# Optimization experiments

Hardware: AMD Instinct MI355X
Metric: run time of the kernel (lower is better)

Reference implementation:

```python
import jax, jax.numpy as jnp
import numpy as np

D_MODEL = 1024
HEADS = 16
D_K = D_MODEL // HEADS
B, S = 2, 2048


def setup_inputs() -> dict:
    key = jax.random.key(0)
    ks = jax.random.split(key, 11)
    sc = 1.0 / np.sqrt(D_MODEL)
    return {
        "q": jax.random.normal(ks[0], (B, S, D_MODEL), jnp.float32),
        "k": jax.random.normal(ks[1], (B, S, D_MODEL), jnp.float32),
        "v": jax.random.normal(ks[2], (B, S, D_MODEL), jnp.float32),
        "Wq": jax.random.normal(ks[3], (D_MODEL, D_MODEL), jnp.float32) * sc,
        "bq": jnp.zeros((D_MODEL,), jnp.float32),
        "Wk": jax.random.normal(ks[4], (D_MODEL, D_MODEL), jnp.float32) * sc,
        "bk": jnp.zeros((D_MODEL,), jnp.float32),
        "Wv": jax.random.normal(ks[5], (D_MODEL, D_MODEL), jnp.float32) * sc,
        "bv": jnp.zeros((D_MODEL,), jnp.float32),
        "Wo": jax.random.normal(ks[6], (D_MODEL, D_MODEL), jnp.float32) * sc,
        "bo": jnp.zeros((D_MODEL,), jnp.float32),
    }


def reference(q, k, v, Wq, bq, Wk, bk, Wv, bv, Wo, bo):
    bs = q.shape[0]
    # linear projections then split heads: [B,S,D] -> [B,H,S,Dk]
    def proj(x, W, b):
        y = x @ W.T + b
        return y.reshape(bs, -1, HEADS, D_K).transpose(0, 2, 1, 3)

    qh = proj(q, Wq, bq)
    kh = proj(k, Wk, bk)
    vh = proj(v, Wv, bv)
    # scores: [B,H,Sq,Sk] -- full attention matrix as in the original
    scores = jnp.einsum("bhqd,bhkd->bhqk", qh, kh) / jnp.sqrt(
        jnp.asarray(D_K, jnp.float32))
    attn = jax.nn.softmax(scores, axis=-1)
    # dropout is identity in eval/reference mode
    out = jnp.einsum("bhqk,bhkd->bhqd", attn, vh)
    concat = out.transpose(0, 2, 1, 3).reshape(bs, -1, D_MODEL)
    return concat @ Wo.T + bo
```

## Files before the change

### kernel.cpp

```cpp
#include <hip/hip_runtime.h>
#include <hip/hip_bf16.h>

typedef __attribute__((ext_vector_type(8))) short bf16x8;
typedef __attribute__((ext_vector_type(4))) float f32x4;
typedef __attribute__((ext_vector_type(16))) float f32x16;

#define DM   1024
#define SEQ  2048
#define NB   2
#define NH   16
#define MR   (NB*SEQ)

#define SMK  (MR*DM)
#define W1M  (DM*DM)

#define QSCALE 0.18033688011112042f

#define OFF_QB  ((size_t)0)
#define OFF_KB  ((size_t)SMK)
#define OFF_WQB ((size_t)(3*(size_t)SMK))
#define OFF_WO  ((size_t)(3*(size_t)SMK + 3*(size_t)W1M))
#define OFF_QP  ((size_t)(3*(size_t)SMK + 4*(size_t)W1M))
#define OFF_KP  ((size_t)(4*(size_t)SMK + 4*(size_t)W1M))
#define OFF_VP  ((size_t)(5*(size_t)SMK + 4*(size_t)W1M))
#define OFF_CC  ((size_t)0)

__device__ __forceinline__ unsigned short f2bf(float f) {
  union { __hip_bfloat16 b; unsigned short u; } cv;
  cv.b = __float2bfloat16(f);
  return cv.u;
}

__device__ __forceinline__ unsigned int cvtpk_bf16(float lo, float hi) {
  unsigned int r;
  asm("v_cvt_pk_bf16_f32 %0, %1, %2" : "=v"(r) : "v"(lo), "v"(hi));
  return r;
}

__device__ __forceinline__ void plane32_swap(unsigned int& a, unsigned int& b) {
  asm("v_permlane32_swap_b32 %0, %1" : "+v"(a), "+v"(b));
}

__global__ __launch_bounds__(256) void cvt_all(const float* __restrict__ wq,
                                               const float* __restrict__ wk,
                                               const float* __restrict__ wo,
                                               const float* __restrict__ v,
                                               unsigned short* __restrict__ ws) {
  int i = blockIdx.x * 256 + threadIdx.x;
  const float* src;
  unsigned short* dst;
  int j;
  if (i < 3 * (W1M / 4)) {
    int z = i >> 18;
    j = i & ((W1M / 4) - 1);
    src = (z == 0) ? wq : ((z == 1) ? wk : wo);
    dst = ws + ((z == 2) ? OFF_WO : OFF_WQB + (size_t)z * W1M);
  } else {
    j = i - 3 * (W1M / 4);
    src = v;
    dst = ws + OFF_KB;
  }
  float4 val = reinterpret_cast<const float4*>(src)[j];
  ushort4 o;
  o.x = f2bf(val.x); o.y = f2bf(val.y); o.z = f2bf(val.z); o.w = f2bf(val.w);
  reinterpret_cast<ushort4*>(dst)[j] = o;
}

__device__ __forceinline__ void gload_lds16(const void* g, void* l) {
  __builtin_amdgcn_global_load_lds(
      (const __attribute__((address_space(1))) unsigned int*)g,
      (__attribute__((address_space(3))) unsigned int*)l,
      16, 0, 0);
}

template<bool BIAS_ROW>
__device__ __forceinline__ void gemm_hyb2_body(unsigned short* __restrict__ As,
                                               unsigned short* __restrict__ Bs,
                                               const float* __restrict__ A,
                                               const unsigned short* __restrict__ B,
                                               const float* __restrict__ bias,
                                               unsigned short* __restrict__ C,
                                               int N, int K, float scale,
                                               int brow, int bcol) {
  const int tid  = threadIdx.x;
  const int lane = tid & 63;
  const int w    = tid >> 6;
  const int wr   = w >> 1, wc = w & 1;

  f32x4 acc[4][4];
#pragma unroll
  for (int m = 0; m < 4; m++)
#pragma unroll
    for (int n = 0; n < 4; n++) acc[m][n] = (f32x4){0.f, 0.f, 0.f, 0.f};

  const int srow = lane >> 2;
  const int scol = (lane & 3) * 8;

  f32x4 ra0[2][2], ra1[2][2];

  auto loadA = [&](int k0, f32x4 (&fa)[2][2]) {
#pragma unroll
    for (int i = 0; i < 2; i++) {
      const float* pa = A + (size_t)(brow + (w + i * 4) * 16 + srow) * K + k0 + scol;
      fa[i][0] = *(const f32x4*)pa;
      fa[i][1] = *(const f32x4*)(pa + 4);
    }
  };
  auto commitA = [&](int buf, f32x4 (&fa)[2][2]) {
#pragma unroll
    for (int i = 0; i < 2; i++) {
      union { unsigned int u[4]; bf16x8 v8; } ua;
#pragma unroll
      for (int j = 0; j < 2; j++) {
        ua.u[2 * j]     = cvtpk_bf16(fa[i][j][0], fa[i][j][1]);
        ua.u[2 * j + 1] = cvtpk_bf16(fa[i][j][2], fa[i][j][3]);
      }
      *(bf16x8*)((char*)As + (size_t)buf * 8192 + (w + i * 4) * 1024 + lane * 16) = ua.v8;
    }
  };
  auto stageB = [&](int buf, int k0) {
#pragma unroll
    for (int c = w; c < 8; c += 4)
      gload_lds16(B + (size_t)(bcol + c * 16 + srow) * K + k0 + scol,
                  (char*)Bs + (size_t)buf * 8192 + c * 1024);
  };

  const int nk = K / 32;

  loadA(0, ra0);
  commitA(0, ra0);
  loadA(32, ra1);
  stageB(0, 0);
  loadA(64, ra0);

  const int lrow_a = wr * 64 + (lane & 15);
  const int lrow_b = wc * 64 + (lane & 15);
  const int lcol   = (lane >> 4) * 8;

  auto iter = [&](int kt, f32x4 (&rs)[2][2]) {
    if (kt + 2 < nk) asm volatile("s_waitcnt vmcnt(4) lgkmcnt(0)" ::: "memory");
    else             asm volatile("s_waitcnt vmcnt(0) lgkmcnt(0)" ::: "memory");
    __builtin_amdgcn_s_barrier();
    __builtin_amdgcn_sched_barrier(0);
    int buf = kt & 1;
    bf16x8 a[4], b[4];
#pragma unroll
    for (int m = 0; m < 4; m++)
      a[m] = *(const bf16x8*)&As[(size_t)buf * 4096 + (lrow_a + m * 16) * 32 + lcol];
#pragma unroll
    for (int n = 0; n < 4; n++)
      b[n] = *(const bf16x8*)&Bs[(size_t)buf * 4096 + (lrow_b + n * 16) * 32 + lcol];
    if (kt + 1 < nk) {
      commitA(buf ^ 1, rs);
      stageB(buf ^ 1, (kt + 1) * 32);
    }
    if (kt + 3 < nk) loadA((kt + 3) * 32, rs);
    __builtin_amdgcn_s_setprio(1);
#pragma unroll
    for (int m = 0; m < 4; m++)
#pragma unroll
      for (int n = 0; n < 4; n++)
        acc[m][n] = __builtin_amdgcn_mfma_f32_16x16x32_bf16(a[m], b[n], acc[m][n], 0, 0, 0);
    __builtin_amdgcn_s_setprio(0);
  };

  for (int kt = 0; kt < nk; kt += 2) {
    iter(kt,     ra1);
    iter(kt + 1, ra0);
  }

  const int crow0 = brow + wr * 64;
  const int ccol0 = bcol + wc * 64;
  const int rsub  = (lane >> 4) * 4;
  const int csub  = lane & 15;
#pragma unroll
  for (int m = 0; m < 4; m++)
#pragma unroll
    for (int n = 0; n < 4; n++) {
      int col = ccol0 + n * 16 + csub;
      float bcol_v = BIAS_ROW ? 0.f : bias[col];
#pragma unroll
      for (int qq = 0; qq < 4; qq++) {
        int row = crow0 + m * 16 + rsub + qq;
        float bb = BIAS_ROW ? bias[row] : bcol_v;
        C[(size_t)row * N + col] = f2bf((acc[m][n][qq] + bb) * scale);
      }
    }
}

__global__ __launch_bounds__(256, 3) void gemm_qkv(const float* __restrict__ q,
                                                   const float* __restrict__ k,
                                                   const float* __restrict__ Wv,
                                                   unsigned short* ws,
                                                   const float* __restrict__ bq,
                                                   const float* __restrict__ bk,
                                                   const float* __restrict__ bv) {
  __shared__ unsigned short As[2 * 128 * 32];
  __shared__ unsigned short Bs[2 * 128 * 32];
  const int i  = blockIdx.x;
  const int x  = i & 7;
  const int r  = i >> 3;
  const int pm = r >> 3;
  const int bx = r & 7;
  const int p  = x * 12 + pm;
  const int z  = p >> 5;
  const int by = p & 31;
  if (z < 2) {
    gemm_hyb2_body<false>(As, Bs,
                          z ? k : q, ws + OFF_WQB + (size_t)z * W1M, z ? bk : bq,
                          ws + OFF_QP + (size_t)z * SMK,
                          DM, DM, z ? 1.f : QSCALE, by * 128, bx * 128);
  } else {
    gemm_hyb2_body<true>(As, Bs,
                         Wv, ws + OFF_KB, bv,
                         ws + OFF_VP,
                         MR, DM, 1.f, bx * 128, by * 128);
  }
}

__device__ __forceinline__ void gemm_out_body(unsigned short* __restrict__ As,
                                              unsigned short* __restrict__ Bs,
                                              const unsigned short* __restrict__ A,
                                              const unsigned short* __restrict__ Bt,
                                              const float* __restrict__ bias,
                                              float* __restrict__ Cv,
                                              int N, int K,
                                              int brow, int bcol) {
  constexpr int BM = 64, BN = 128;
  const int tid  = threadIdx.x;
  const int lane = tid & 63;
  const int w    = tid >> 6;
  const int wr   = w >> 1, wc = w & 1;

  f32x4 acc[2][4];
#pragma unroll
  for (int m = 0; m < 2; m++)
#pragma unroll
    for (int n = 0; n < 4; n++) acc[m][n] = (f32x4){0.f, 0.f, 0.f, 0.f};

  const int srow = lane >> 2;
  const int scol = (lane & 3) * 8;

  auto stage = [&](int buf, int k0) {
#pragma unroll
    for (int c = w; c < BM / 16; c += 4)
      gload_lds16(A + (size_t)(brow + c * 16 + srow) * K + k0 + scol,
                  (char*)As + (size_t)buf * BM * 64 + c * 1024);
#pragma unroll
    for (int c = w; c < BN / 16; c += 4)
      gload_lds16(Bt + (size_t)(bcol + c * 16 + srow) * K + k0 + scol,
                  (char*)Bs + (size_t)buf * BN * 64 + c * 1024);
  };

  stage(0, 0);
  stage(1, 32);

  const int nk = K / 32;
  const int lrow_a = wr * (BM / 2) + (lane & 15);
  const int lrow_b = wc * (BN / 2) + (lane & 15);
  const int lcol   = (lane >> 4) * 8;

  int b0 = 0;
  for (int kt = 0; kt < nk; ++kt) {
    if (kt + 1 < nk) asm volatile("s_waitcnt vmcnt(3)" ::: "memory");
    else             asm volatile("s_waitcnt vmcnt(0)" ::: "memory");
    __builtin_amdgcn_s_barrier();
    __builtin_amdgcn_sched_barrier(0);
    if (kt + 2 < nk) {
      int bn = b0 + 2; if (bn >= 3) bn -= 3;
      stage(bn, (kt + 2) * 32);
    }
    bf16x8 a[2], b[4];
#pragma unroll
    for (int m = 0; m < 2; m++)
      a[m] = *(const bf16x8*)&As[(size_t)b0 * BM * 32 + (lrow_a + m * 16) * 32 + lcol];
#pragma unroll
    for (int n = 0; n < 4; n++)
      b[n] = *(const bf16x8*)&Bs[(size_t)b0 * BN * 32 + (lrow_b + n * 16) * 32 + lcol];
    __builtin_amdgcn_s_setprio(1);
#pragma unroll
    for (int m = 0; m < 2; m++)
#pragma unroll
      for (int n = 0; n < 4; n++)
        acc[m][n] = __builtin_amdgcn_mfma_f32_16x16x32_bf16(a[m], b[n], acc[m][n], 0, 0, 0);
    __builtin_amdgcn_s_setprio(0);
    b0 = (b0 == 2) ? 0 : b0 + 1;
  }

  const int crow0 = brow + wr * (BM / 2);
  const int ccol0 = bcol + wc * (BN / 2);
  const int rsub  = (lane >> 4) * 4;
  const int csub  = lane & 15;
#pragma unroll
  for (int m = 0; m < 2; m++)
#pragma unroll
    for (int n = 0; n < 4; n++) {
      int col = ccol0 + n * 16 + csub;
      float bv = bias[col];
#pragma unroll
      for (int qq = 0; qq < 4; qq++) {
        int row = crow0 + m * 16 + rsub + qq;
        Cv[(size_t)row * N + col] = acc[m][n][qq] + bv;
      }
    }
}

__global__ __launch_bounds__(256) void gemm_out(const unsigned short* __restrict__ ws,
                                                const float* __restrict__ bo,
                                                float* __restrict__ out) {
  __shared__ unsigned short As[3 * 64 * 32];
  __shared__ unsigned short Bs[3 * 128 * 32];
  const int i  = blockIdx.x;
  const int x  = i & 7;
  const int r  = i >> 3;
  const int pm = r >> 3;
  const int bx = r & 7;
  const int by = x * 8 + pm;
  gemm_out_body(As, Bs,
                ws + OFF_CC, ws + OFF_WO, bo, out,
                DM, DM, by * 64, bx * 128);
}

__global__ __launch_bounds__(512, 4) void flash_attn(unsigned short* ws) {
  __shared__ __align__(16) unsigned char smem[65536];

  const int tid  = threadIdx.x;
  const int lane = tid & 63;
  const int w    = tid >> 6;
  const int s    = w >> 2;
  const int wsub = w & 3;
  const int q    = lane & 31;
  const int hi   = lane >> 5;
  const int swq  = q & 7;
  const int bid  = blockIdx.x;
  const int swzb = (bid & 7) * 64 + (bid >> 3);
  const int qblk = swzb & 15;
  const int bh   = swzb >> 4;
  const int b    = bh >> 4, h = bh & 15;

  const unsigned short* Qp = ws + OFF_QP;
  const unsigned short* Kp = ws + OFF_KP;
  const unsigned short* Vp = ws + OFF_VP;
  unsigned short* CC = ws + OFF_CC;

  const unsigned short* Kg = Kp + (size_t)(b * SEQ) * DM + h * 64;
  const unsigned short* Vg = Vp + (size_t)(h * 64) * MR + (size_t)b * SEQ;

  bf16x8 bqf[4];
  {
    const unsigned short* qrow =
        Qp + (size_t)(b * SEQ + qblk * 128 + wsub * 32 + q) * DM + h * 64;
#pragma unroll
    for (int c = 0; c < 4; c++)
      bqf[c] = *(const bf16x8*)(qrow + c * 16 + hi * 8);
  }

  f32x16 o_acc[2];
#pragma unroll
  for (int dt = 0; dt < 2; dt++)
#pragma unroll
    for (int r = 0; r < 16; r++) o_acc[dt][r] = 0.f;
  float l_run = 0.f;

  auto stage = [&](int buf, int t) {
    const unsigned short* Kt = Kg + (size_t)(s * 16 + t) * 64 * DM;
    const unsigned short* Vt = Vg + (s * 16 + t) * 64;
    char* base = (char*)smem + (size_t)(s * 2 + buf) * 16384;
#pragma unroll
    for (int i = 0; i < 2; i++) {
      int slot = wsub * 128 + i * 64 + lane;
      int srow = slot >> 3;
      int gch  = (slot & 7) ^ (srow & 7);
      gload_lds16(Kt + (size_t)srow * DM + gch * 8, base + slot * 16);
      gload_lds16(Vt + (size_t)srow * MR + gch * 8, base + 8192 + slot * 16);
    }
  };

  stage(0, 0);

  for (int t = 0; t < 16; ++t) {
    int buf = t & 1;
    __syncthreads();
    if (t + 1 < 16) stage(buf ^ 1, t + 1);
    const unsigned short* Kb = (const unsigned short*)(smem + (size_t)(s * 2 + buf) * 16384);
    const unsigned short* Vb = Kb + 4096;

    f32x16 st0, st1;
#pragma unroll
    for (int r = 0; r < 16; r++) { st0[r] = 0.f; st1[r] = 0.f; }
    __builtin_amdgcn_s_setprio(1);
#pragma unroll
    for (int c = 0; c < 4; c++) {
      int ch = (((c << 1) | hi) ^ swq) << 3;
      bf16x8 ak0 = *(const bf16x8*)&Kb[q * 64 + ch];
      bf16x8 ak1 = *(const bf16x8*)&Kb[(32 + q) * 64 + ch];
      st0 = __builtin_amdgcn_mfma_f32_32x32x16_bf16(ak0, bqf[c], st0, 0, 0, 0);
      st1 = __builtin_amdgcn_mfma_f32_32x32x16_bf16(ak1, bqf[c], st1, 0, 0, 0);
    }
    __builtin_amdgcn_s_setprio(0);

    unsigned int pk0[8], pk1[8];
    float lt = 0.f;
#pragma unroll
    for (int p = 0; p < 8; p++) {
      float a0 = __builtin_amdgcn_exp2f(st0[2 * p]);
      float a1 = __builtin_amdgcn_exp2f(st0[2 * p + 1]);
      float b0 = __builtin_amdgcn_exp2f(st1[2 * p]);
      float b1 = __builtin_amdgcn_exp2f(st1[2 * p + 1]);
      lt += (a0 + a1) + (b0 + b1);
      pk0[p] = cvtpk_bf16(a0, a1);
      pk1[p] = cvtpk_bf16(b0, b1);
    }
    l_run += lt;

    plane32_swap(pk0[0], pk0[2]); plane32_swap(pk0[1], pk0[3]);
    plane32_swap(pk0[4], pk0[6]); plane32_swap(pk0[5], pk0[7]);
    plane32_swap(pk1[0], pk1[2]); plane32_swap(pk1[1], pk1[3]);
    plane32_swap(pk1[4], pk1[6]); plane32_swap(pk1[5], pk1[7]);

    __builtin_amdgcn_s_setprio(1);
#pragma unroll
    for (int t4 = 0; t4 < 4; t4++) {
      union { unsigned int u[4]; bf16x8 v; } pb;
      const unsigned int* src = (t4 < 2) ? pk0 : pk1;
      pb.u[0] = src[(t4 & 1) * 4 + 0];
      pb.u[1] = src[(t4 & 1) * 4 + 1];
      pb.u[2] = src[(t4 & 1) * 4 + 2];
      pb.u[3] = src[(t4 & 1) * 4 + 3];
      int ch = (((t4 << 1) | hi) ^ swq) << 3;
#pragma unroll
      for (int dt = 0; dt < 2; dt++) {
        bf16x8 av = *(const bf16x8*)&Vb[(dt * 32 + q) * 64 + ch];
        o_acc[dt] = __builtin_amdgcn_mfma_f32_32x32x16_bf16(av, pb.v, o_acc[dt], 0, 0, 0);
      }
    }
    __builtin_amdgcn_s_setprio(0);
  }

  __syncthreads();
  float* scr = (float*)smem;
  float lsum = l_run + __shfl_xor(l_run, 32, 64);
  if (s == 1) {
    int idx = (wsub * 64 + lane) * 33;
#pragma unroll
    for (int dt = 0; dt < 2; dt++)
#pragma unroll
      for (int r = 0; r < 16; r++) scr[idx + dt * 16 + r] = o_acc[dt][r];
    scr[idx + 32] = lsum;
  }
  __syncthreads();
  if (s == 0) {
    int idx = (wsub * 64 + lane) * 33;
#pragma unroll
    for (int dt = 0; dt < 2; dt++)
#pragma unroll
      for (int r = 0; r < 16; r++) o_acc[dt][r] += scr[idx + dt * 16 + r];
    float l = lsum + scr[idx + 32];
    float inv = 1.f / l;

    int qg = b * SEQ + qblk * 128 + wsub * 32 + q;
    unsigned short* crow = CC + (size_t)qg * DM + h * 64;
#pragma unroll
    for (int dt = 0; dt < 2; dt++)
#pragma unroll
      for (int rq = 0; rq < 4; rq++) {
        ushort4 o;
        o.x = f2bf(o_acc[dt][4 * rq + 0] * inv);
        o.y = f2bf(o_acc[dt][4 * rq + 1] * inv);
        o.z = f2bf(o_acc[dt][4 * rq + 2] * inv);
        o.w = f2bf(o_acc[dt][4 * rq + 3] * inv);
        *(ushort4*)&crow[dt * 32 + rq * 8 + hi * 4] = o;
      }
  }
}

extern "C" void kernel_launch(void* const* d_in, const int* in_sizes, int n_in,
                              void* d_out, int out_size, void* d_ws, size_t ws_size,
                              hipStream_t stream) {
  const float* q  = (const float*)d_in[0];
  const float* k  = (const float*)d_in[1];
  const float* v  = (const float*)d_in[2];
  const float* Wq = (const float*)d_in[3];
  const float* bq = (const float*)d_in[4];
  const float* Wk = (const float*)d_in[5];
  const float* bk = (const float*)d_in[6];
  const float* Wv = (const float*)d_in[7];
  const float* bv = (const float*)d_in[8];
  const float* Wo = (const float*)d_in[9];
  const float* bo = (const float*)d_in[10];

  unsigned short* ws = (unsigned short*)d_ws;
  float* out = (float*)d_out;

  cvt_all<<<dim3((3 * (W1M / 4) + SMK / 4) / 256), dim3(256), 0, stream>>>(
      Wq, Wk, Wo, v, ws);

  gemm_qkv<<<dim3(768), dim3(256), 0, stream>>>(q, k, Wv, ws, bq, bk, bv);

  flash_attn<<<dim3(512), dim3(512), 0, stream>>>(ws);

  gemm_out<<<dim3(512), dim3(256), 0, stream>>>(ws, bo, out);
}
```

Baseline: 110.6 us.

## Fuse Wo fp32-to-bf16 conversion into output projection GEMM B-tile staging

Drops the separate Wo conversion from the cvt_all prep kernel. gemm_out now reads Wo as fp32 straight into registers, converts it to bf16 with v_cvt_pk_bf16_f32, and writes it to LDS through a register-prefetched double buffer, while A stays on the direct global-to-LDS path. This removes one 1M-element conversion pass and its bf16 write and read-back. In exchange, gemm_out reads twice as many bytes for B per tile, every block repeats the conversion, and the pipeline drops from triple to double buffering with added VGPR pressure.

```diff
diff --git a/kernel.cpp b/kernel.cpp
--- a/kernel.cpp
+++ b/kernel.cpp
@@ -19,7 +19,6 @@
 #define OFF_QB  ((size_t)0)
 #define OFF_KB  ((size_t)SMK)
 #define OFF_WQB ((size_t)(3*(size_t)SMK))
-#define OFF_WO  ((size_t)(3*(size_t)SMK + 3*(size_t)W1M))
 #define OFF_QP  ((size_t)(3*(size_t)SMK + 4*(size_t)W1M))
 #define OFF_KP  ((size_t)(4*(size_t)SMK + 4*(size_t)W1M))
 #define OFF_VP  ((size_t)(5*(size_t)SMK + 4*(size_t)W1M))
@@ -43,20 +42,19 @@
 
 __global__ __launch_bounds__(256) void cvt_all(const float* __restrict__ wq,
                                                const float* __restrict__ wk,
-                                               const float* __restrict__ wo,
                                                const float* __restrict__ v,
                                                unsigned short* __restrict__ ws) {
   int i = blockIdx.x * 256 + threadIdx.x;
   const float* src;
   unsigned short* dst;
   int j;
-  if (i < 3 * (W1M / 4)) {
+  if (i < 2 * (W1M / 4)) {
     int z = i >> 18;
     j = i & ((W1M / 4) - 1);
-    src = (z == 0) ? wq : ((z == 1) ? wk : wo);
-    dst = ws + ((z == 2) ? OFF_WO : OFF_WQB + (size_t)z * W1M);
+    src = z ? wk : wq;
+    dst = ws + OFF_WQB + (size_t)z * W1M;
   } else {
-    j = i - 3 * (W1M / 4);
+    j = i - 2 * (W1M / 4);
     src = v;
     dst = ws + OFF_KB;
   }
@@ -221,12 +219,11 @@
 __device__ __forceinline__ void gemm_out_body(unsigned short* __restrict__ As,
                                               unsigned short* __restrict__ Bs,
                                               const unsigned short* __restrict__ A,
-                                              const unsigned short* __restrict__ Bt,
+                                              const float* __restrict__ Bw,
                                               const float* __restrict__ bias,
                                               float* __restrict__ Cv,
                                               int N, int K,
                                               int brow, int bcol) {
-  constexpr int BM = 64, BN = 128;
   const int tid  = threadIdx.x;
   const int lane = tid & 63;
   const int w    = tid >> 6;
@@ -241,42 +238,63 @@
   const int srow = lane >> 2;
   const int scol = (lane & 3) * 8;
 
-  auto stage = [&](int buf, int k0) {
-#pragma unroll
-    for (int c = w; c < BM / 16; c += 4)
-      gload_lds16(A + (size_t)(brow + c * 16 + srow) * K + k0 + scol,
-                  (char*)As + (size_t)buf * BM * 64 + c * 1024);
-#pragma unroll
-    for (int c = w; c < BN / 16; c += 4)
-      gload_lds16(Bt + (size_t)(bcol + c * 16 + srow) * K + k0 + scol,
-                  (char*)Bs + (size_t)buf * BN * 64 + c * 1024);
-  };
-
-  stage(0, 0);
-  stage(1, 32);
+  f32x4 rb0[2][2], rb1[2][2];
+
+  auto loadB = [&](int k0, f32x4 (&fb)[2][2]) {
+#pragma unroll
+    for (int i = 0; i < 2; i++) {
+      const float* pb = Bw + (size_t)(bcol + (w + i * 4) * 16 + srow) * K + k0 + scol;
+      fb[i][0] = *(const f32x4*)pb;
+      fb[i][1] = *(const f32x4*)(pb + 4);
+    }
+  };
+  auto commitB = [&](int buf, f32x4 (&fb)[2][2]) {
+#pragma unroll
+    for (int i = 0; i < 2; i++) {
+      union { unsigned int u[4]; bf16x8 v8; } ub;
+#pragma unroll
+      for (int j = 0; j < 2; j++) {
+        ub.u[2 * j]     = cvtpk_bf16(fb[i][j][0], fb[i][j][1]);
+        ub.u[2 * j + 1] = cvtpk_bf16(fb[i][j][2], fb[i][j][3]);
+      }
+      *(bf16x8*)((char*)Bs + (size_t)buf * 8192 + (w + i * 4) * 1024 + lane * 16) = ub.v8;
+    }
+  };
+  auto stageA = [&](int buf, int k0) {
+    gload_lds16(A + (size_t)(brow + w * 16 + srow) * K + k0 + scol,
+                (char*)As + (size_t)buf * 4096 + w * 1024);
+  };
 
   const int nk = K / 32;
-  const int lrow_a = wr * (BM / 2) + (lane & 15);
-  const int lrow_b = wc * (BN / 2) + (lane & 15);
+
+  loadB(0, rb0);
+  commitB(0, rb0);
+  loadB(32, rb1);
+  stageA(0, 0);
+  loadB(64, rb0);
+
+  const int lrow_a = wr * 32 + (lane & 15);
+  const int lrow_b = wc * 64 + (lane & 15);
   const int lcol   = (lane >> 4) * 8;
 
-  int b0 = 0;
-  for (int kt = 0; kt < nk; ++kt) {
-    if (kt + 1 < nk) asm volatile("s_waitcnt vmcnt(3)" ::: "memory");
-    else             asm volatile("s_waitcnt vmcnt(0)" ::: "memory");
+  auto iter = [&](int kt, f32x4 (&rs)[2][2]) {
+    if (kt + 2 < nk) asm volatile("s_waitcnt vmcnt(4) lgkmcnt(0)" ::: "memory");
+    else             asm volatile("s_waitcnt vmcnt(0) lgkmcnt(0)" ::: "memory");
     __builtin_amdgcn_s_barrier();
     __builtin_amdgcn_sched_barrier(0);
-    if (kt + 2 < nk) {
-      int bn = b0 + 2; if (bn >= 3) bn -= 3;
-      stage(bn, (kt + 2) * 32);
-    }
+    int buf = kt & 1;
     bf16x8 a[2], b[4];
 #pragma unroll
     for (int m = 0; m < 2; m++)
-      a[m] = *(const bf16x8*)&As[(size_t)b0 * BM * 32 + (lrow_a + m * 16) * 32 + lcol];
+      a[m] = *(const bf16x8*)&As[(size_t)buf * 2048 + (lrow_a + m * 16) * 32 + lcol];
 #pragma unroll
     for (int n = 0; n < 4; n++)
-      b[n] = *(const bf16x8*)&Bs[(size_t)b0 * BN * 32 + (lrow_b + n * 16) * 32 + lcol];
+      b[n] = *(const bf16x8*)&Bs[(size_t)buf * 4096 + (lrow_b + n * 16) * 32 + lcol];
+    if (kt + 1 < nk) {
+      commitB(buf ^ 1, rs);
+      stageA(buf ^ 1, (kt + 1) * 32);
+    }
+    if (kt + 3 < nk) loadB((kt + 3) * 32, rs);
     __builtin_amdgcn_s_setprio(1);
 #pragma unroll
     for (int m = 0; m < 2; m++)
@@ -284,11 +302,15 @@
       for (int n = 0; n < 4; n++)
         acc[m][n] = __builtin_amdgcn_mfma_f32_16x16x32_bf16(a[m], b[n], acc[m][n], 0, 0, 0);
     __builtin_amdgcn_s_setprio(0);
-    b0 = (b0 == 2) ? 0 : b0 + 1;
-  }
-
-  const int crow0 = brow + wr * (BM / 2);
-  const int ccol0 = bcol + wc * (BN / 2);
+  };
+
+  for (int kt = 0; kt < nk; kt += 2) {
+    iter(kt,     rb1);
+    iter(kt + 1, rb0);
+  }
+
+  const int crow0 = brow + wr * 32;
+  const int ccol0 = bcol + wc * 64;
   const int rsub  = (lane >> 4) * 4;
   const int csub  = lane & 15;
 #pragma unroll
@@ -305,11 +327,12 @@
     }
 }
 
-__global__ __launch_bounds__(256) void gemm_out(const unsigned short* __restrict__ ws,
-                                                const float* __restrict__ bo,
-                                                float* __restrict__ out) {
-  __shared__ unsigned short As[3 * 64 * 32];
-  __shared__ unsigned short Bs[3 * 128 * 32];
+__global__ __launch_bounds__(256, 3) void gemm_out(const unsigned short* __restrict__ ws,
+                                                   const float* __restrict__ Wo,
+                                                   const float* __restrict__ bo,
+                                                   float* __restrict__ out) {
+  __shared__ unsigned short As[2 * 64 * 32];
+  __shared__ unsigned short Bs[2 * 128 * 32];
   const int i  = blockIdx.x;
   const int x  = i & 7;
   const int r  = i >> 3;
@@ -317,7 +340,7 @@
   const int bx = r & 7;
   const int by = x * 8 + pm;
   gemm_out_body(As, Bs,
-                ws + OFF_CC, ws + OFF_WO, bo, out,
+                ws + OFF_CC, Wo, bo, out,
                 DM, DM, by * 64, bx * 128);
 }
 
@@ -492,12 +515,12 @@
   unsigned short* ws = (unsigned short*)d_ws;
   float* out = (float*)d_out;
 
-  cvt_all<<<dim3((3 * (W1M / 4) + SMK / 4) / 256), dim3(256), 0, stream>>>(
-      Wq, Wk, Wo, v, ws);
+  cvt_all<<<dim3((2 * (W1M / 4) + SMK / 4) / 256), dim3(256), 0, stream>>>(
+      Wq, Wk, v, ws);
 
   gemm_qkv<<<dim3(768), dim3(256), 0, stream>>>(q, k, Wv, ws, bq, bk, bv);
 
   flash_attn<<<dim3(512), dim3(512), 0, stream>>>(ws);
 
-  gemm_out<<<dim3(512), dim3(256), 0, stream>>>(ws, bo, out);
-}
+  gemm_out<<<dim3(512), dim3(256), 0, stream>>>(ws, Wo, bo, out);
+}
```

New measurement: 113.4 us. +2.6%, slower.
